# Kernel optimization log

Hardware: AMD Instinct MI355X
Metric: run time of the kernel (lower is better)

## Reference

```python
import jax, jax.numpy as jnp
import numpy as np

B, S, HID, H = 2, 2048, 2048, 16
D = HID // H  # 128 head dim
SCALE = 1.0 / np.sqrt(D)


def setup_inputs() -> dict:
    key = jax.random.key(0)
    ks = jax.random.split(key, 10)
    w = lambda k, shp: (jax.random.normal(k, shp, jnp.float32) * 0.02)
    x = jax.random.normal(ks[0], (B, S, HID), jnp.float32)
    mask = jnp.tril(jnp.ones((S, S), jnp.bool_))[None, None]  # causal [1,1,S,S]
    return {
        "x": x,
        "mask": mask,
        "Wq": w(ks[1], (HID, HID)), "bq": w(ks[2], (HID,)),
        "Wk": w(ks[3], (D, HID)),   "bk": w(ks[4], (D,)),
        "Wv": w(ks[5], (D, HID)),   "bv": w(ks[6], (D,)),
        "Wo": w(ks[7], (HID, HID)), "bo": w(ks[8], (HID,)),
    }


def reference(x, mask, Wq, bq, Wk, bk, Wv, bv, Wo, bo):
    b, s, _ = x.shape
    # projections (torch Linear: x @ W.T + b)
    q = (x @ Wq.T + bq).reshape(b, s, H, D).transpose(0, 2, 1, 3)  # [B,H,S,D]
    k = x @ Wk.T + bk  # [B,S,D] single KV head
    v = x @ Wv.T + bv  # [B,S,D]
    scores = jnp.einsum("bhqd,bkd->bhqk", q, k) * SCALE  # [B,H,S,S]
    scores = jnp.where(mask, scores, -jnp.inf)
    attn = jax.nn.softmax(scores, axis=-1)
    out = jnp.einsum("bhqk,bkd->bhqd", attn, v)  # [B,H,S,D]
    out = out.transpose(0, 2, 1, 3).reshape(b, s, HID)
    return out @ Wo.T + bo
```

## Files before the change

### kernel.cpp

```cpp
#include <hip/hip_runtime.h>


#define S_LEN 2048
#define HID_  2048
#define D_    128
#define NQKV  2304

typedef __attribute__((ext_vector_type(8))) short bf16x8;
typedef __attribute__((ext_vector_type(4))) float f32x4;
typedef __attribute__((ext_vector_type(16))) float f32x16;

__device__ __forceinline__ unsigned short f2b(float f) {
  union { float f; unsigned int u; } a; a.f = f;
  unsigned int u = a.u;
  return (unsigned short)((u + 0x7fffu + ((u >> 16) & 1u)) >> 16);
}

__device__ __forceinline__ float b2f(unsigned short s) {
  union { unsigned int u; float f; } a; a.u = ((unsigned int)s) << 16;
  return a.f;
}

__device__ __forceinline__ void load_lds16(const void* g, void* l) {
  __builtin_amdgcn_global_load_lds(
      (const __attribute__((address_space(1))) void*)g,
      (__attribute__((address_space(3))) void*)l, 16, 0, 0);
}

__device__ __forceinline__ f32x4 mfma16(bf16x8 a, bf16x8 b, f32x4 c) {
  return __builtin_amdgcn_mfma_f32_16x16x32_bf16(a, b, c, 0, 0, 0);
}

__device__ __forceinline__ f32x16 mfma32(bf16x8 a, bf16x8 b, f32x16 c) {
  return __builtin_amdgcn_mfma_f32_32x32x16_bf16(a, b, c, 0, 0, 0);
}

__device__ __forceinline__ unsigned int cvtpk(float lo, float hi) {
  unsigned int r;
  asm volatile("v_cvt_pk_bf16_f32 %0, %1, %2" : "=v"(r) : "v"(lo), "v"(hi));
  return r;
}


__global__ void cast_f32_bf16_k(const float* __restrict__ in,
                                unsigned short* __restrict__ out, int n4) {
  const int idx = blockIdx.x * 256 + threadIdx.x;
  if (idx < n4) {
    const float4 v = ((const float4*)in)[idx];
    ushort4 o;
    o.x = f2b(v.x); o.y = f2b(v.y); o.z = f2b(v.z); o.w = f2b(v.w);
    ((ushort4*)out)[idx] = o;
  }
}

__global__ void build_wcat_k(const float* __restrict__ Wq,
                             const float* __restrict__ Wk,
                             const float* __restrict__ Wv,
                             const float* __restrict__ bq,
                             const float* __restrict__ bk,
                             const float* __restrict__ bv,
                             unsigned short* __restrict__ Wcat,
                             float* __restrict__ bcat,
                             float* __restrict__ Kmax) {
  const int idx = blockIdx.x * 256 + threadIdx.x;
  const int i = idx * 4;
  const int row = i >> 11;
  const int col = i & 2047;
  const float* src;
  if (row < 2048)      src = Wq + (size_t)row * 2048 + col;
  else if (row < 2176) src = Wk + (size_t)(row - 2048) * 2048 + col;
  else                 src = Wv + (size_t)(row - 2176) * 2048 + col;
  const float4 v = *(const float4*)src;
  ushort4 o;
  o.x = f2b(v.x); o.y = f2b(v.y); o.z = f2b(v.z); o.w = f2b(v.w);
  *(ushort4*)(Wcat + i) = o;
  if (idx < NQKV)
    bcat[idx] = (idx < 2048) ? bq[idx] : (idx < 2176) ? bk[idx - 2048] : bv[idx - 2176];
  if (idx < 2) Kmax[idx] = 0.f;
}

__global__ __launch_bounds__(256)
void transpose_v(const unsigned short* __restrict__ QKV,
                 unsigned short* __restrict__ Vt) {
  __shared__ unsigned short tile[64][136];
  const int tid = threadIdx.x;
  const int s0  = blockIdx.x * 64;
  const int b   = blockIdx.y;
  const int row = tid >> 2;
  const int cb  = (tid & 3) * 32;
  const unsigned short* src = QKV + (size_t)(b * S_LEN + s0 + row) * NQKV + 2176 + cb;
#pragma unroll
  for (int i = 0; i < 4; ++i)
    *(bf16x8*)&tile[row][cb + i * 8] = *(const bf16x8*)(src + i * 8);
  __syncthreads();
  const int d  = tid >> 1;
  const int sc = (tid & 1) * 32;
  unsigned short* dst = Vt + ((size_t)b * D_ + d) * S_LEN + s0 + sc;
#pragma unroll
  for (int i = 0; i < 4; ++i) {
    bf16x8 vv;
#pragma unroll
    for (int e = 0; e < 8; ++e) vv[e] = tile[sc + i * 8 + e][d];
    *(bf16x8*)(dst + i * 8) = vv;
  }
}

__global__ __launch_bounds__(256)
void kmax_k(const unsigned short* __restrict__ QKV, float* __restrict__ Kmax) {
  __shared__ float red[256];
  const int tid = threadIdx.x;
  const int b = blockIdx.x >> 3;
  const int s = (blockIdx.x & 7) * 256 + tid;
  const unsigned short* kp = QKV + (size_t)(b * S_LEN + s) * NQKV + 2048;
  float sum = 0.f;
#pragma unroll
  for (int i = 0; i < 16; ++i) {
    bf16x8 v = *(const bf16x8*)(kp + i * 8);
#pragma unroll
    for (int e = 0; e < 8; ++e) { const float f = b2f((unsigned short)v[e]); sum += f * f; }
  }
  red[tid] = sum;
  __syncthreads();
  for (int off = 128; off > 0; off >>= 1) {
    if (tid < off) red[tid] = fmaxf(red[tid], red[tid + off]);
    __syncthreads();
  }
  if (tid == 0) atomicMax((unsigned int*)(Kmax + b), __float_as_uint(red[0]));
}


template <int OUT_F32, int NJ>
__global__ __launch_bounds__(512, 2)
void gemm_nt2(const unsigned short* __restrict__ A,
              const unsigned short* __restrict__ Bm,
              const float* __restrict__ bias,
              void* __restrict__ Cv,
              int N, int K) {
  constexpr int BN = 64 * NJ;
  __shared__ __align__(16) char As[3][128 * 128];
  __shared__ __align__(16) char Bs[3][BN * 128];

  const int tid  = threadIdx.x;
  const int lane = tid & 63;
  const int wv   = tid >> 6;
  const int wr   = wv >> 2;
  const int wc   = wv & 3;
  const int g    = lane >> 4, r = lane & 15;

  const int nwg  = gridDim.x;
  const int bid  = blockIdx.x;
  const int sbid = (bid & 7) * (nwg >> 3) + (bid >> 3);
  const int nx   = N / BN;
  const int m0   = (sbid / nx) * 128;
  const int n0   = (sbid % nx) * BN;
  const int NT   = K >> 6;

  const size_t Kb = (size_t)K * 2;
  const char* Ab = (const char*)A + (size_t)m0 * Kb;
  const char* Bb = (const char*)Bm + (size_t)n0 * Kb;

#define STAGE_A(bufi, t)                                                       \
  {                                                                            \
    const int kb_ = (t) * 128;                                                 \
    _Pragma("unroll")                                                          \
    for (int i_ = 0; i_ < 2; ++i_) {                                           \
      const int ch_ = tid + 512 * i_;                                          \
      const int rr_ = ch_ >> 3;                                                \
      const int sl_ = (ch_ & 7) ^ (rr_ & 7);                                   \
      load_lds16(Ab + (size_t)rr_ * Kb + kb_ + sl_ * 16, As[bufi] + ch_ * 16); \
    }                                                                          \
  }
#define STAGE_B(bufi, t)                                                       \
  {                                                                            \
    const int kb_ = (t) * 128;                                                 \
    _Pragma("unroll")                                                          \
    for (int i_ = 0; i_ < NJ; ++i_) {                                          \
      const int ch_ = tid + 512 * i_;                                          \
      const int rr_ = ch_ >> 3;                                                \
      const int sl_ = (ch_ & 7) ^ (rr_ & 7);                                   \
      load_lds16(Bb + (size_t)rr_ * Kb + kb_ + sl_ * 16, Bs[bufi] + ch_ * 16); \
    }                                                                          \
  }

  f32x4 acc[4][NJ] = {};
  const int s0 = ((g ^ (r & 7)) << 4);
  const int s1 = (((4 | g) ^ (r & 7)) << 4);

  STAGE_A(0, 0) STAGE_B(0, 0) STAGE_A(1, 1) STAGE_B(1, 1)

  asm volatile("s_waitcnt vmcnt(%0)" :: "i"(NJ + 2) : "memory");
  __builtin_amdgcn_s_barrier();
  __builtin_amdgcn_sched_barrier(0);

  for (int t = 0; t < NT; ++t) {
    const char* as = As[t % 3];
    const char* bs = Bs[t % 3];
    const int nb = (t + 2) % 3;
    const bool pf = (t + 2 < NT);

    bf16x8 af[4], bfr[NJ];
#pragma unroll
    for (int i = 0; i < 4; ++i)
      af[i] = *(const bf16x8*)(as + ((wr * 64 + i * 16 + r) << 7) + s0);
#pragma unroll
    for (int j = 0; j < NJ; ++j)
      bfr[j] = *(const bf16x8*)(bs + ((wc * 16 * NJ + j * 16 + r) << 7) + s0);
    if (pf) STAGE_A(nb, t + 2)
    __builtin_amdgcn_s_barrier();
    __builtin_amdgcn_sched_barrier(0);
    asm volatile("s_waitcnt lgkmcnt(0)" ::: "memory");
    __builtin_amdgcn_sched_barrier(0);
    __builtin_amdgcn_s_setprio(1);
#pragma unroll
    for (int i = 0; i < 4; ++i)
#pragma unroll
      for (int j = 0; j < NJ; ++j)
        acc[i][j] = mfma16(af[i], bfr[j], acc[i][j]);
    __builtin_amdgcn_s_setprio(0);
    __builtin_amdgcn_sched_barrier(0);

#pragma unroll
    for (int i = 0; i < 4; ++i)
      af[i] = *(const bf16x8*)(as + ((wr * 64 + i * 16 + r) << 7) + s1);
#pragma unroll
    for (int j = 0; j < NJ; ++j)
      bfr[j] = *(const bf16x8*)(bs + ((wc * 16 * NJ + j * 16 + r) << 7) + s1);
    if (pf) STAGE_B(nb, t + 2)
    __builtin_amdgcn_s_barrier();
    __builtin_amdgcn_sched_barrier(0);
    asm volatile("s_waitcnt lgkmcnt(0)" ::: "memory");
    __builtin_amdgcn_sched_barrier(0);
    __builtin_amdgcn_s_setprio(1);
#pragma unroll
    for (int i = 0; i < 4; ++i)
#pragma unroll
      for (int j = 0; j < NJ; ++j)
        acc[i][j] = mfma16(af[i], bfr[j], acc[i][j]);
    __builtin_amdgcn_s_setprio(0);

    if (pf) { asm volatile("s_waitcnt vmcnt(%0)" :: "i"(NJ + 2) : "memory"); }
    else    { asm volatile("s_waitcnt vmcnt(0)" ::: "memory"); }
    __builtin_amdgcn_s_barrier();
    __builtin_amdgcn_sched_barrier(0);
  }

#pragma unroll
  for (int i = 0; i < 4; ++i) {
    const int row = m0 + wr * 64 + i * 16 + g * 4;
#pragma unroll
    for (int j = 0; j < NJ; ++j) {
      const int col = n0 + wc * 16 * NJ + j * 16 + r;
      const float bb = bias[col];
#pragma unroll
      for (int e = 0; e < 4; ++e) {
        const float v = acc[i][j][e] + bb;
        if (OUT_F32) ((float*)Cv)[(size_t)(row + e) * N + col] = v;
        else ((unsigned short*)Cv)[(size_t)(row + e) * N + col] = f2b(v);
      }
    }
  }
#undef STAGE_A
#undef STAGE_B
}


__global__ __launch_bounds__(256, 2)
void mqa_attn(const unsigned short* __restrict__ QKV,
              const unsigned short* __restrict__ Vt,
              const float* __restrict__ Kmax,
              unsigned short* __restrict__ Ob) {
  __shared__ __align__(16) char Ks[2][64 * 256];
  __shared__ __align__(16) char Vs[2][64 * 256];

  const int tid  = threadIdx.x;
  const int lane = tid & 63;
  const int wv   = tid >> 6;
  const int ln   = lane & 31;
  const int hi   = lane >> 5;
  const int x    = blockIdx.x;
  const int lo   = x & 255;
  const int b    = lo >> 7;
  const int hq   = (lo >> 5) & 3;
  const int qtl  = lo & 31;
  const int qt   = (x < 256) ? qtl : 63 - qtl;
  const int h    = hq * 4 + wv;
  const int qw   = qt * 32;
  const int nt   = (qt >> 1) + 1;

  bf16x8 qf[8];
  {
    const unsigned short* qp =
        QKV + (size_t)(b * S_LEN + qw + ln) * NQKV + h * D_ + hi * 8;
#pragma unroll
    for (int ch = 0; ch < 8; ++ch) qf[ch] = *(const bf16x8*)(qp + ch * 16);
  }

  const float sscale = 0.08838834764831845f * 1.4426950408889634f;
  float qn2 = 0.f;
#pragma unroll
  for (int ch = 0; ch < 8; ++ch)
#pragma unroll
    for (int e = 0; e < 8; ++e) {
      const float qv = b2f((unsigned short)qf[ch][e]);
      qn2 += qv * qv;
    }
  qn2 += __shfl_xor(qn2, 32);
  const float m0c = sqrtf(qn2) * sqrtf(Kmax[b]) * sscale + 1.0f;

  const char* kbc = (const char*)(QKV + (size_t)(b * S_LEN) * NQKV + 2048);
  const char* vbc = (const char*)(Vt + (size_t)b * D_ * S_LEN);

  f32x16 acc[4] = {};
  float accl = 0.f;

#define STAGE(bufi, t)                                                         \
  {                                                                            \
    const int kv0_ = (t) * 64;                                                 \
    _Pragma("unroll")                                                          \
    for (int i_ = 0; i_ < 4; ++i_) {                                           \
      const int ch_ = tid + 256 * i_;                                          \
      const int kr_ = ch_ >> 4;                                                \
      const int kg_ = (ch_ & 15) ^ (kr_ & 15);                                 \
      load_lds16(kbc + (size_t)(kv0_ + kr_) * (NQKV * 2) + kg_ * 16,           \
                 Ks[bufi] + ch_ * 16);                                         \
      const int vg_ = (ch_ & 15) ^ (kr_ & 15);                                 \
      const int vd_ = kr_ * 2 + (vg_ >> 3);                                    \
      load_lds16(vbc + (size_t)vd_ * (S_LEN * 2) + kv0_ * 2 + (vg_ & 7) * 16,  \
                 Vs[bufi] + ch_ * 16);                                         \
    }                                                                          \
  }

  STAGE(0, 0);
  int cur = 0;

  for (int t = 0; t < nt; ++t) {
    __syncthreads();
    if (t + 1 < nt) STAGE(cur ^ 1, t + 1);

    const char* ksb = Ks[cur];
    const char* vsb = Vs[cur];
    const int kv0 = t * 64;
    const bool last = (t == nt - 1);
    const bool doUp = (kv0 + 32 <= qw + 31);
    cur ^= 1;

    f32x16 sA = {}, sB = {};
    __builtin_amdgcn_s_setprio(1);
#pragma unroll
    for (int ch = 0; ch < 8; ++ch) {
      const int slot0 = (2 * ch + hi) ^ (ln & 15);
      const bf16x8 kf0 = *(const bf16x8*)(ksb + ln * 256 + slot0 * 16);
      sA = mfma32(kf0, qf[ch], sA);
      if (doUp) {
        const bf16x8 kf1 = *(const bf16x8*)(ksb + (32 + ln) * 256 + slot0 * 16);
        sB = mfma32(kf1, qf[ch], sB);
      }
    }
    __builtin_amdgcn_s_setprio(0);

    bf16x8 pa0, pa1, pa2, pa3;
    float p[16];

#define SOFTMAX(sv, kvtbase)                                                   \
    _Pragma("unroll")                                                          \
    for (int rr = 0; rr < 16; ++rr) {                                          \
      float e = sv[rr] * sscale - m0c;                                         \
      if (last) {                                                              \
        const int kva = (kvtbase) + (rr & 3) + 8 * (rr >> 2) + 4 * hi;         \
        e = (kva <= qw + ln) ? e : -__builtin_inff();                          \
      }                                                                        \
      const float pv_ = __builtin_amdgcn_exp2f(e);                             \
      p[rr] = pv_; accl += pv_;                                                \
    }

#define PACK2(fa, fb)                                                          \
    {                                                                          \
      const unsigned int A0 = cvtpk(p[0], p[1]),   A1 = cvtpk(p[2], p[3]);     \
      const unsigned int B0 = cvtpk(p[4], p[5]),   B1 = cvtpk(p[6], p[7]);     \
      const unsigned int C0 = cvtpk(p[8], p[9]),   C1 = cvtpk(p[10], p[11]);   \
      const unsigned int D0 = cvtpk(p[12], p[13]), D1 = cvtpk(p[14], p[15]);   \
      unsigned int X0 = hi ? A0 : B0, X1 = hi ? A1 : B1;                       \
      unsigned int Y0 = hi ? C0 : D0, Y1 = hi ? C1 : D1;                       \
      X0 = (unsigned int)__shfl_xor((int)X0, 32);                              \
      X1 = (unsigned int)__shfl_xor((int)X1, 32);                              \
      Y0 = (unsigned int)__shfl_xor((int)Y0, 32);                              \
      Y1 = (unsigned int)__shfl_xor((int)Y1, 32);                              \
      union { unsigned int w[4]; bf16x8 v; } ua, ub;                           \
      ua.w[0] = hi ? X0 : A0; ua.w[1] = hi ? X1 : A1;                          \
      ua.w[2] = hi ? B0 : X0; ua.w[3] = hi ? B1 : X1;                          \
      ub.w[0] = hi ? Y0 : C0; ub.w[1] = hi ? Y1 : C1;                          \
      ub.w[2] = hi ? D0 : Y0; ub.w[3] = hi ? D1 : Y1;                          \
      fa = ua.v; fb = ub.v;                                                    \
    }

    SOFTMAX(sA, kv0)
    PACK2(pa0, pa1)
    if (doUp) {
      SOFTMAX(sB, kv0 + 32)
      PACK2(pa2, pa3)
    }

    __builtin_amdgcn_s_setprio(1);
#pragma unroll
    for (int dt = 0; dt < 4; ++dt) {
      const int vrow = dt * 16 + (ln >> 1);
      const int gb   = (ln & 1) << 3;
      {
        const int sl = (gb + 0 + hi) ^ (vrow & 15);
        const bf16x8 vf = *(const bf16x8*)(vsb + vrow * 256 + sl * 16);
        acc[dt] = mfma32(pa0, vf, acc[dt]);
      }
      {
        const int sl = (gb + 2 + hi) ^ (vrow & 15);
        const bf16x8 vf = *(const bf16x8*)(vsb + vrow * 256 + sl * 16);
        acc[dt] = mfma32(pa1, vf, acc[dt]);
      }
      if (doUp) {
        {
          const int sl = (gb + 4 + hi) ^ (vrow & 15);
          const bf16x8 vf = *(const bf16x8*)(vsb + vrow * 256 + sl * 16);
          acc[dt] = mfma32(pa2, vf, acc[dt]);
        }
        {
          const int sl = (gb + 6 + hi) ^ (vrow & 15);
          const bf16x8 vf = *(const bf16x8*)(vsb + vrow * 256 + sl * 16);
          acc[dt] = mfma32(pa3, vf, acc[dt]);
        }
      }
    }
    __builtin_amdgcn_s_setprio(0);
#undef SOFTMAX
#undef PACK2
  }

  const float lf = accl + __shfl_xor(accl, 32);
  const float linv = 1.0f / lf;
  unsigned short* ob = Ob + (size_t)(b * S_LEN + qw) * HID_ + h * D_ + ln;
#pragma unroll
  for (int rr = 0; rr < 16; ++rr) {
    const int qr = (rr & 3) + 8 * (rr >> 2) + 4 * hi;
    const float li = __shfl(linv, qr);
#pragma unroll
    for (int dt = 0; dt < 4; ++dt)
      ob[(size_t)qr * HID_ + dt * 32] = f2b(acc[dt][rr] * li);
  }
#undef STAGE
}


extern "C" void kernel_launch(void* const* d_in, const int* in_sizes, int n_in,
                              void* d_out, int out_size, void* d_ws, size_t ws_size,
                              hipStream_t stream) {
  (void)in_sizes; (void)n_in; (void)out_size; (void)ws_size;
  const float* x  = (const float*)d_in[0];
  const float* Wq = (const float*)d_in[2];
  const float* bq = (const float*)d_in[3];
  const float* Wk = (const float*)d_in[4];
  const float* bk = (const float*)d_in[5];
  const float* Wv = (const float*)d_in[6];
  const float* bv = (const float*)d_in[7];
  const float* Wo = (const float*)d_in[8];
  const float* bo = (const float*)d_in[9];
  float* out = (float*)d_out;

  char* p = (char*)d_ws;
  unsigned short* xb   = (unsigned short*)p;  p += (size_t)4096 * 2048 * 2;
  unsigned short* Wcat = (unsigned short*)p;  p += (size_t)2304 * 2048 * 2;
  float*          bcat = (float*)p;           p += 16384;
  unsigned short* Wob  = (unsigned short*)p;  p += (size_t)2048 * 2048 * 2;
  unsigned short* QKV  = (unsigned short*)p;  p += (size_t)4096 * 2304 * 2;
  unsigned short* Vt   = (unsigned short*)p;  p += (size_t)2 * 128 * 2048 * 2;
  float*          Kmax = (float*)p;           p += 64;
  unsigned short* Ob   = xb;

  cast_f32_bf16_k<<<8192, 256, 0, stream>>>(x, xb, 2097152);
  build_wcat_k<<<4608, 256, 0, stream>>>(Wq, Wk, Wv, bq, bk, bv, Wcat, bcat, Kmax);
  cast_f32_bf16_k<<<4096, 256, 0, stream>>>(Wo, Wob, 1048576);
  gemm_nt2<0, 3><<<384, 512, 0, stream>>>(xb, Wcat, bcat, QKV, 2304, 2048);
  transpose_v<<<dim3(32, 2), 256, 0, stream>>>(QKV, Vt);
  kmax_k<<<16, 256, 0, stream>>>(QKV, Kmax);
  mqa_attn<<<512, 256, 0, stream>>>(QKV, Vt, Kmax, Ob);
  gemm_nt2<1, 4><<<256, 512, 0, stream>>>(Ob, Wob, bo, out, 2048, 2048);
}
```

Baseline: 199.2 us.

## Triple-buffer 32-row KV tiles with explicit vmcnt waits in MQA attention

Shrinks the attention KV tile from 64 to 32 rows and switches from double to triple buffering. Prefetch now runs two tiles ahead, and the single __syncthreads is replaced by explicit s_waitcnt vmcnt plus a raw s_barrier. Smaller LDS use allows launch_bounds of 3 blocks per CU and removes the doUp half-tile branch. In exchange there are twice as many loop iterations and barriers, less MFMA work per sync, and correctness depends on the hand-counted vmcnt values.

```diff
diff --git a/kernel.cpp b/kernel.cpp
--- a/kernel.cpp
+++ b/kernel.cpp
@@ -264,13 +264,13 @@
 }
 
 
-__global__ __launch_bounds__(256, 2)
+__global__ __launch_bounds__(256, 3)
 void mqa_attn(const unsigned short* __restrict__ QKV,
               const unsigned short* __restrict__ Vt,
               const float* __restrict__ Kmax,
               unsigned short* __restrict__ Ob) {
-  __shared__ __align__(16) char Ks[2][64 * 256];
-  __shared__ __align__(16) char Vs[2][64 * 256];
+  __shared__ __align__(16) char Ks[3][32 * 256];
+  __shared__ __align__(16) char Vs[3][32 * 256];
 
   const int tid  = threadIdx.x;
   const int lane = tid & 63;
@@ -285,7 +285,7 @@
   const int qt   = (x < 256) ? qtl : 63 - qtl;
   const int h    = hq * 4 + wv;
   const int qw   = qt * 32;
-  const int nt   = (qt >> 1) + 1;
+  const int nt   = qt + 1;
 
   bf16x8 qf[8];
   {
@@ -315,122 +315,94 @@
 
 #define STAGE(bufi, t)                                                         \
   {                                                                            \
-    const int kv0_ = (t) * 64;                                                 \
+    const int kv0_ = (t) * 32;                                                 \
     _Pragma("unroll")                                                          \
-    for (int i_ = 0; i_ < 4; ++i_) {                                           \
+    for (int i_ = 0; i_ < 2; ++i_) {                                           \
       const int ch_ = tid + 256 * i_;                                          \
-      const int kr_ = ch_ >> 4;                                                \
-      const int kg_ = (ch_ & 15) ^ (kr_ & 15);                                 \
-      load_lds16(kbc + (size_t)(kv0_ + kr_) * (NQKV * 2) + kg_ * 16,           \
+      const int rr_ = ch_ >> 4;                                                \
+      const int gk_ = (ch_ & 15) ^ (rr_ & 15);                                 \
+      load_lds16(kbc + (size_t)(kv0_ + rr_) * (NQKV * 2) + gk_ * 16,           \
                  Ks[bufi] + ch_ * 16);                                         \
-      const int vg_ = (ch_ & 15) ^ (kr_ & 15);                                 \
-      const int vd_ = kr_ * 2 + (vg_ >> 3);                                    \
-      load_lds16(vbc + (size_t)vd_ * (S_LEN * 2) + kv0_ * 2 + (vg_ & 7) * 16,  \
+      const int gv_ = (ch_ & 15) ^ (rr_ & 15);                                 \
+      const int vd_ = rr_ * 4 + (gv_ >> 2);                                    \
+      load_lds16(vbc + (size_t)vd_ * (S_LEN * 2) + kv0_ * 2 + (gv_ & 3) * 16,  \
                  Vs[bufi] + ch_ * 16);                                         \
     }                                                                          \
   }
 
-  STAGE(0, 0);
-  int cur = 0;
+  __builtin_amdgcn_sched_barrier(0);
+  STAGE(0, 0) STAGE(1, 1)
+  asm volatile("s_waitcnt vmcnt(4)" ::: "memory");
+  __builtin_amdgcn_s_barrier();
+  __builtin_amdgcn_sched_barrier(0);
 
   for (int t = 0; t < nt; ++t) {
-    __syncthreads();
-    if (t + 1 < nt) STAGE(cur ^ 1, t + 1);
-
-    const char* ksb = Ks[cur];
-    const char* vsb = Vs[cur];
-    const int kv0 = t * 64;
+    const char* ksb = Ks[t % 3];
+    const char* vsb = Vs[t % 3];
+    const int kv0 = t * 32;
     const bool last = (t == nt - 1);
-    const bool doUp = (kv0 + 32 <= qw + 31);
-    cur ^= 1;
-
-    f32x16 sA = {}, sB = {};
+    const bool pf = (t + 2 < nt);
+    if (pf) STAGE((t + 2) % 3, t + 2)
+
+    f32x16 sA = {};
     __builtin_amdgcn_s_setprio(1);
 #pragma unroll
     for (int ch = 0; ch < 8; ++ch) {
       const int slot0 = (2 * ch + hi) ^ (ln & 15);
       const bf16x8 kf0 = *(const bf16x8*)(ksb + ln * 256 + slot0 * 16);
       sA = mfma32(kf0, qf[ch], sA);
-      if (doUp) {
-        const bf16x8 kf1 = *(const bf16x8*)(ksb + (32 + ln) * 256 + slot0 * 16);
-        sB = mfma32(kf1, qf[ch], sB);
+    }
+    __builtin_amdgcn_s_setprio(0);
+
+    bf16x8 pa0, pa1;
+    float p[16];
+#pragma unroll
+    for (int rr = 0; rr < 16; ++rr) {
+      float e = sA[rr] * sscale - m0c;
+      if (last) {
+        const int kva = kv0 + (rr & 3) + 8 * (rr >> 2) + 4 * hi;
+        e = (kva <= qw + ln) ? e : -__builtin_inff();
       }
+      const float pv_ = __builtin_amdgcn_exp2f(e);
+      p[rr] = pv_; accl += pv_;
+    }
+    {
+      const unsigned int A0 = cvtpk(p[0], p[1]),   A1 = cvtpk(p[2], p[3]);
+      const unsigned int B0 = cvtpk(p[4], p[5]),   B1 = cvtpk(p[6], p[7]);
+      const unsigned int C0 = cvtpk(p[8], p[9]),   C1 = cvtpk(p[10], p[11]);
+      const unsigned int D0 = cvtpk(p[12], p[13]), D1 = cvtpk(p[14], p[15]);
+      unsigned int X0 = hi ? A0 : B0, X1 = hi ? A1 : B1;
+      unsigned int Y0 = hi ? C0 : D0, Y1 = hi ? C1 : D1;
+      X0 = (unsigned int)__shfl_xor((int)X0, 32);
+      X1 = (unsigned int)__shfl_xor((int)X1, 32);
+      Y0 = (unsigned int)__shfl_xor((int)Y0, 32);
+      Y1 = (unsigned int)__shfl_xor((int)Y1, 32);
+      union { unsigned int w[4]; bf16x8 v; } ua, ub;
+      ua.w[0] = hi ? X0 : A0; ua.w[1] = hi ? X1 : A1;
+      ua.w[2] = hi ? B0 : X0; ua.w[3] = hi ? B1 : X1;
+      ub.w[0] = hi ? Y0 : C0; ub.w[1] = hi ? Y1 : C1;
+      ub.w[2] = hi ? D0 : Y0; ub.w[3] = hi ? D1 : Y1;
+      pa0 = ua.v; pa1 = ub.v;
+    }
+
+    __builtin_amdgcn_s_setprio(1);
+#pragma unroll
+    for (int dt = 0; dt < 4; ++dt) {
+      const int vr = dt * 8 + (ln >> 2);
+      const char* base = vsb + vr * 256;
+      const int sl0 = (((ln & 3) << 2) + hi) ^ (vr & 15);
+      acc[dt] = mfma32(pa0, *(const bf16x8*)(base + sl0 * 16), acc[dt]);
+      const int sl1 = (((ln & 3) << 2) + 2 + hi) ^ (vr & 15);
+      acc[dt] = mfma32(pa1, *(const bf16x8*)(base + sl1 * 16), acc[dt]);
     }
     __builtin_amdgcn_s_setprio(0);
 
-    bf16x8 pa0, pa1, pa2, pa3;
-    float p[16];
-
-#define SOFTMAX(sv, kvtbase)                                                   \
-    _Pragma("unroll")                                                          \
-    for (int rr = 0; rr < 16; ++rr) {                                          \
-      float e = sv[rr] * sscale - m0c;                                         \
-      if (last) {                                                              \
-        const int kva = (kvtbase) + (rr & 3) + 8 * (rr >> 2) + 4 * hi;         \
-        e = (kva <= qw + ln) ? e : -__builtin_inff();                          \
-      }                                                                        \
-      const float pv_ = __builtin_amdgcn_exp2f(e);                             \
-      p[rr] = pv_; accl += pv_;                                                \
-    }
-
-#define PACK2(fa, fb)                                                          \
-    {                                                                          \
-      const unsigned int A0 = cvtpk(p[0], p[1]),   A1 = cvtpk(p[2], p[3]);     \
-      const unsigned int B0 = cvtpk(p[4], p[5]),   B1 = cvtpk(p[6], p[7]);     \
-      const unsigned int C0 = cvtpk(p[8], p[9]),   C1 = cvtpk(p[10], p[11]);   \
-      const unsigned int D0 = cvtpk(p[12], p[13]), D1 = cvtpk(p[14], p[15]);   \
-      unsigned int X0 = hi ? A0 : B0, X1 = hi ? A1 : B1;                       \
-      unsigned int Y0 = hi ? C0 : D0, Y1 = hi ? C1 : D1;                       \
-      X0 = (unsigned int)__shfl_xor((int)X0, 32);                              \
-      X1 = (unsigned int)__shfl_xor((int)X1, 32);                              \
-      Y0 = (unsigned int)__shfl_xor((int)Y0, 32);                              \
-      Y1 = (unsigned int)__shfl_xor((int)Y1, 32);                              \
-      union { unsigned int w[4]; bf16x8 v; } ua, ub;                           \
-      ua.w[0] = hi ? X0 : A0; ua.w[1] = hi ? X1 : A1;                          \
-      ua.w[2] = hi ? B0 : X0; ua.w[3] = hi ? B1 : X1;                          \
-      ub.w[0] = hi ? Y0 : C0; ub.w[1] = hi ? Y1 : C1;                          \
-      ub.w[2] = hi ? D0 : Y0; ub.w[3] = hi ? D1 : Y1;                          \
-      fa = ua.v; fb = ub.v;                                                    \
-    }
-
-    SOFTMAX(sA, kv0)
-    PACK2(pa0, pa1)
-    if (doUp) {
-      SOFTMAX(sB, kv0 + 32)
-      PACK2(pa2, pa3)
-    }
-
-    __builtin_amdgcn_s_setprio(1);
-#pragma unroll
-    for (int dt = 0; dt < 4; ++dt) {
-      const int vrow = dt * 16 + (ln >> 1);
-      const int gb   = (ln & 1) << 3;
-      {
-        const int sl = (gb + 0 + hi) ^ (vrow & 15);
-        const bf16x8 vf = *(const bf16x8*)(vsb + vrow * 256 + sl * 16);
-        acc[dt] = mfma32(pa0, vf, acc[dt]);
-      }
-      {
-        const int sl = (gb + 2 + hi) ^ (vrow & 15);
-        const bf16x8 vf = *(const bf16x8*)(vsb + vrow * 256 + sl * 16);
-        acc[dt] = mfma32(pa1, vf, acc[dt]);
-      }
-      if (doUp) {
-        {
-          const int sl = (gb + 4 + hi) ^ (vrow & 15);
-          const bf16x8 vf = *(const bf16x8*)(vsb + vrow * 256 + sl * 16);
-          acc[dt] = mfma32(pa2, vf, acc[dt]);
-        }
-        {
-          const int sl = (gb + 6 + hi) ^ (vrow & 15);
-          const bf16x8 vf = *(const bf16x8*)(vsb + vrow * 256 + sl * 16);
-          acc[dt] = mfma32(pa3, vf, acc[dt]);
-        }
-      }
-    }
-    __builtin_amdgcn_s_setprio(0);
-#undef SOFTMAX
-#undef PACK2
+    if (t + 1 < nt) {
+      if (pf) { asm volatile("s_waitcnt vmcnt(4)" ::: "memory"); }
+      else    { asm volatile("s_waitcnt vmcnt(0)" ::: "memory"); }
+      __builtin_amdgcn_s_barrier();
+      __builtin_amdgcn_sched_barrier(0);
+    }
   }
 
   const float lf = accl + __shfl_xor(accl, 32);
```

New measurement: 216.2 us. +8.5%, slower.

## Split long causal attention rows across two KV chunks with a combine pass

Applied to the files above, without the earlier changes.

Query tiles in the second half of the sequence now have their KV range split into two chunks, each handled by a separate workgroup, which raises the grid from 512 to 768 blocks and balances the causal work. Partial unnormalized accumulators and row sums go to a workspace in bf16, and a new combine kernel sums them and normalizes. The split relies on the softmax using a fixed global max (Kmax-based), so the partials can be added without rescaling. The cost is an extra kernel launch, extra global traffic, and bf16 rounding of the partials.

```diff
diff --git a/kernel.cpp b/kernel.cpp
--- a/kernel.cpp
+++ b/kernel.cpp
@@ -268,7 +268,9 @@
 void mqa_attn(const unsigned short* __restrict__ QKV,
               const unsigned short* __restrict__ Vt,
               const float* __restrict__ Kmax,
-              unsigned short* __restrict__ Ob) {
+              unsigned short* __restrict__ Ob,
+              unsigned short* __restrict__ Pacc,
+              float* __restrict__ Pl) {
   __shared__ __align__(16) char Ks[2][64 * 256];
   __shared__ __align__(16) char Vs[2][64 * 256];
 
@@ -278,14 +280,17 @@
   const int ln   = lane & 31;
   const int hi   = lane >> 5;
   const int x    = blockIdx.x;
-  const int lo   = x & 255;
-  const int b    = lo >> 7;
-  const int hq   = (lo >> 5) & 3;
-  const int qtl  = lo & 31;
-  const int qt   = (x < 256) ? qtl : 63 - qtl;
+  const int bhq  = x & 7;
+  const int b    = bhq >> 2;
+  const int hq   = bhq & 3;
+  const int widx = x >> 3;
+  int qt, t0, te, chunk;
+  if (widx < 32)      { qt = 32 + widx; t0 = 0;  te = 16;         chunk = 0; }
+  else if (widx < 64) { qt = 95 - widx; t0 = 16; te = qt / 2 + 1; chunk = 1; }
+  else                { qt = 95 - widx; t0 = 0;  te = qt / 2 + 1; chunk = -1; }
   const int h    = hq * 4 + wv;
   const int qw   = qt * 32;
-  const int nt   = (qt >> 1) + 1;
+  const int lastT = qt / 2;
 
   bf16x8 qf[8];
   {
@@ -330,17 +335,17 @@
     }                                                                          \
   }
 
-  STAGE(0, 0);
+  STAGE(0, t0);
   int cur = 0;
 
-  for (int t = 0; t < nt; ++t) {
+  for (int t = t0; t < te; ++t) {
     __syncthreads();
-    if (t + 1 < nt) STAGE(cur ^ 1, t + 1);
+    if (t + 1 < te) STAGE(cur ^ 1, t + 1);
 
     const char* ksb = Ks[cur];
     const char* vsb = Vs[cur];
     const int kv0 = t * 64;
-    const bool last = (t == nt - 1);
+    const bool last = (t == lastT);
     const bool doUp = (kv0 + 32 <= qw + 31);
     cur ^= 1;
 
@@ -434,17 +439,61 @@
   }
 
   const float lf = accl + __shfl_xor(accl, 32);
-  const float linv = 1.0f / lf;
-  unsigned short* ob = Ob + (size_t)(b * S_LEN + qw) * HID_ + h * D_ + ln;
-#pragma unroll
-  for (int rr = 0; rr < 16; ++rr) {
-    const int qr = (rr & 3) + 8 * (rr >> 2) + 4 * hi;
-    const float li = __shfl(linv, qr);
-#pragma unroll
-    for (int dt = 0; dt < 4; ++dt)
-      ob[(size_t)qr * HID_ + dt * 32] = f2b(acc[dt][rr] * li);
+
+  if (chunk < 0) {
+    const float linv = 1.0f / lf;
+    unsigned short* ob = Ob + (size_t)(b * S_LEN + qw) * HID_ + h * D_ + ln;
+#pragma unroll
+    for (int rr = 0; rr < 16; ++rr) {
+      const int qr = (rr & 3) + 8 * (rr >> 2) + 4 * hi;
+      const float li = __shfl(linv, qr);
+#pragma unroll
+      for (int dt = 0; dt < 4; ++dt)
+        ob[(size_t)qr * HID_ + dt * 32] = f2b(acc[dt][rr] * li);
+    }
+  } else {
+    const int slot = ((chunk * 2 + b) * 16 + h) * 32 + (qt - 32);
+    unsigned short* pa = Pacc + (size_t)slot * 32 * 128 + ln;
+#pragma unroll
+    for (int rr = 0; rr < 16; ++rr) {
+      const int qr = (rr & 3) + 8 * (rr >> 2) + 4 * hi;
+#pragma unroll
+      for (int dt = 0; dt < 4; ++dt)
+        pa[qr * 128 + dt * 32] = f2b(acc[dt][rr]);
+    }
+    if (hi == 0) Pl[slot * 32 + ln] = lf;
   }
 #undef STAGE
+}
+
+__global__ __launch_bounds__(256)
+void combine_k(const unsigned short* __restrict__ Pacc,
+               const float* __restrict__ Pl,
+               unsigned short* __restrict__ Ob) {
+  const int x  = blockIdx.x;
+  const int qs = x & 31;
+  const int h  = (x >> 5) & 15;
+  const int b  = x >> 9;
+  const int tid = threadIdx.x;
+  const int q  = tid >> 3;
+  const int dp = (tid & 7) * 16;
+  const int s0 = (b * 16 + h) * 32 + qs;
+  const int s1 = ((2 + b) * 16 + h) * 32 + qs;
+  const float inv = 1.0f / (Pl[s0 * 32 + q] + Pl[s1 * 32 + q]);
+  const unsigned short* a0 = Pacc + ((size_t)s0 * 32 + q) * 128 + dp;
+  const unsigned short* a1 = Pacc + ((size_t)s1 * 32 + q) * 128 + dp;
+  unsigned short* ob =
+      Ob + (size_t)(b * S_LEN + (32 + qs) * 32 + q) * HID_ + h * D_ + dp;
+  const bf16x8 v0a = *(const bf16x8*)a0, v0b = *(const bf16x8*)(a0 + 8);
+  const bf16x8 v1a = *(const bf16x8*)a1, v1b = *(const bf16x8*)(a1 + 8);
+  bf16x8 oa, obv;
+#pragma unroll
+  for (int e = 0; e < 8; ++e) {
+    oa[e]  = (short)f2b((b2f((unsigned short)v0a[e]) + b2f((unsigned short)v1a[e])) * inv);
+    obv[e] = (short)f2b((b2f((unsigned short)v0b[e]) + b2f((unsigned short)v1b[e])) * inv);
+  }
+  *(bf16x8*)ob = oa;
+  *(bf16x8*)(ob + 8) = obv;
 }
 
 
@@ -471,6 +520,8 @@
   unsigned short* QKV  = (unsigned short*)p;  p += (size_t)4096 * 2304 * 2;
   unsigned short* Vt   = (unsigned short*)p;  p += (size_t)2 * 128 * 2048 * 2;
   float*          Kmax = (float*)p;           p += 64;
+  unsigned short* Pacc = (unsigned short*)p;  p += (size_t)2048 * 32 * 128 * 2;
+  float*          Pl   = (float*)p;           p += (size_t)2048 * 32 * 4;
   unsigned short* Ob   = xb;
 
   cast_f32_bf16_k<<<8192, 256, 0, stream>>>(x, xb, 2097152);
@@ -479,6 +530,7 @@
   gemm_nt2<0, 3><<<384, 512, 0, stream>>>(xb, Wcat, bcat, QKV, 2304, 2048);
   transpose_v<<<dim3(32, 2), 256, 0, stream>>>(QKV, Vt);
   kmax_k<<<16, 256, 0, stream>>>(QKV, Kmax);
-  mqa_attn<<<512, 256, 0, stream>>>(QKV, Vt, Kmax, Ob);
+  mqa_attn<<<768, 256, 0, stream>>>(QKV, Vt, Kmax, Ob, Pacc, Pl);
+  combine_k<<<1024, 256, 0, stream>>>(Pacc, Pl, Ob);
   gemm_nt2<1, 4><<<256, 512, 0, stream>>>(Ob, Wob, bo, out, 2048, 2048);
 }
```

After: 191.2 us. 4.0% less time.
